# Performance work log

Measured on AMD Instinct MI355X. Metric: run time of the kernel, lower is better.

## Reference

```python
import jax, jax.numpy as jnp
import numpy as np

B, D, H, HD, P, O, K = 256, 1024, 8, 128, 2048, 1024, 4
HID = H * HD
EPS = 1e-5


def setup_inputs() -> dict:
    key = jax.random.key(0)
    ks = jax.random.split(key, 16)

    def w(k, shape, fan_in):
        return jax.random.normal(k, shape, jnp.float32) / np.sqrt(fan_in).astype(np.float32)

    return dict(
        seq=jax.random.normal(ks[0], (B, D), jnp.float32),
        c_tm1=jnp.zeros((B, H, HD, HD), jnp.float32),
        n_tm1=jnp.ones((B, H, HD), jnp.float32),
        m_tm1=jnp.zeros((B, H), jnp.float32),
        ln_g=jnp.ones((D,), jnp.float32), ln_b=jnp.zeros((D,), jnp.float32),
        gn_g=jnp.ones((HID,), jnp.float32), gn_b=jnp.zeros((HID,), jnp.float32),
        W_upl=w(ks[1], (P, D), D), b_upl=jnp.zeros((P,), jnp.float32),
        W_upr=w(ks[2], (HID, D), D), b_upr=jnp.zeros((HID,), jnp.float32),
        W_down=w(ks[3], (D, HID), HID), b_down=jnp.zeros((D,), jnp.float32),
        W_last=w(ks[4], (O, D), D), b_last=jnp.zeros((O,), jnp.float32),
        conv_w=w(ks[5], (K,), K), conv_b=jnp.zeros((), jnp.float32),
        W_skip=w(ks[6], (HID, P), P),
        W_i=w(ks[7], (H, P), P), b_i=jnp.zeros((H,), jnp.float32),
        W_f=w(ks[8], (H, P), P), b_f=jnp.zeros((H,), jnp.float32),
        W_o=w(ks[9], (HID, P), P), b_o=jnp.zeros((HID,), jnp.float32),
        W_q=w(ks[10], (HID, P), P), b_q=jnp.zeros((HID,), jnp.float32),
        W_k=w(ks[11], (HID, P), P), b_k=jnp.zeros((HID,), jnp.float32),
        W_v=w(ks[12], (HID, P), P), b_v=jnp.zeros((HID,), jnp.float32),
    )


def reference(seq, c_tm1, n_tm1, m_tm1, ln_g, ln_b, gn_g, gn_b,
              W_upl, b_upl, W_upr, b_upr, W_down, b_down, W_last, b_last,
              conv_w, conv_b, W_skip, W_i, b_i, W_f, b_f, W_o, b_o,
              W_q, b_q, W_k, b_k, W_v, b_v):
    b = seq.shape[0]
    h, hd = c_tm1.shape[1], c_tm1.shape[2]

    # input LayerNorm
    mu = jnp.mean(seq, -1, keepdims=True)
    var = jnp.var(seq, -1, keepdims=True)
    x_n = (seq - mu) * jax.lax.rsqrt(var + EPS) * ln_g + ln_b

    x_t = x_n @ W_upl.T + b_upl            # [b, P]
    r_t = x_n @ W_upr.T + b_upr            # [b, HID]

    # causal conv over the feature axis (in=out=1 channel), left pad K-1
    k_sz = conv_w.shape[0]
    p = x_t.shape[1]
    xp = jnp.pad(x_t, ((0, 0), (k_sz - 1, 0)))
    x_c = conv_b + sum(conv_w[j] * xp[:, j:j + p] for j in range(k_sz))
    x_c = jax.nn.silu(x_c)                 # [b, P]

    q_t = (x_c @ W_q.T + b_q).reshape(b, h, hd)
    k_t = ((x_c @ W_k.T + b_k) / np.sqrt(hd).astype(np.float32)).reshape(b, h, hd)
    v_t = (x_t @ W_v.T + b_v).reshape(b, h, hd)

    i_t = x_c @ W_i.T + b_i                # [b, h]
    f_t = x_c @ W_f.T + b_f                # [b, h]
    o_t = jax.nn.sigmoid(x_t @ W_o.T + b_o)  # [b, HID]

    # stabilized exponential gating
    m_t = jnp.maximum(f_t + m_tm1, i_t)
    i_g = jnp.exp(i_t - m_t)
    f_g = jnp.exp(f_t - m_t + m_tm1)

    # matrix-memory covariance update
    c_t = f_g[:, :, None, None] * c_tm1 + i_g[:, :, None, None] * jnp.einsum('bhd,bhp->bhdp', v_t, k_t)
    n_t = f_g[:, :, None] * n_tm1 + i_g[:, :, None] * k_t

    num = jnp.einsum('bhdp,bhp->bhd', c_t, q_t)
    den = jnp.maximum(jnp.einsum('bhd,bhd->bh', n_t, q_t), 1.0)
    h_t = o_t * (num / den[:, :, None]).reshape(b, h * hd)

    # GroupNorm(head_num groups) over hidden
    hg = h_t.reshape(b, h, hd)
    gmu = jnp.mean(hg, -1, keepdims=True)
    gvar = jnp.var(hg, -1, keepdims=True)
    hn = ((hg - gmu) * jax.lax.rsqrt(gvar + EPS)).reshape(b, h * hd) * gn_g + gn_b

    out = hn + x_c @ W_skip.T              # 1x1 conv skip == matmul
    out = out * jax.nn.silu(r_t)
    out = out @ W_down.T + b_down
    final = (out + x_n) @ W_last.T + b_last
    return final, c_t, n_t, m_t
```

## Files before the change

### kernel.cpp

```cpp
#include <hip/hip_runtime.h>
#include <cstdint>
#include <cstddef>

#define LN_EPS 1e-5f

typedef float  f32x4  __attribute__((ext_vector_type(4)));
typedef __bf16 bf16x8 __attribute__((ext_vector_type(8)));
typedef unsigned short u16x4 __attribute__((ext_vector_type(4)));

__device__ __forceinline__ float block_sum(float v, volatile float* red) {
#pragma unroll
  for (int o = 32; o > 0; o >>= 1) v += __shfl_down(v, o, 64);
  const int lane = threadIdx.x & 63, w = threadIdx.x >> 6;
  __syncthreads();
  if (lane == 0) red[w] = v;
  __syncthreads();
  return red[0] + red[1] + red[2] + red[3];
}

__global__ __launch_bounds__(256)
void k_ln(const float* __restrict__ seq, const float* __restrict__ g,
          const float* __restrict__ b, float* __restrict__ xn) {
  __shared__ float red[8];
  const int row = blockIdx.x, t = threadIdx.x;
  const f32x4 x = ((const f32x4*)(seq + (size_t)row * 1024))[t];
  float s  = x[0] + x[1] + x[2] + x[3];
  float s2 = x[0]*x[0] + x[1]*x[1] + x[2]*x[2] + x[3]*x[3];
#pragma unroll
  for (int o = 32; o > 0; o >>= 1) { s += __shfl_down(s, o, 64); s2 += __shfl_down(s2, o, 64); }
  const int lane = t & 63, w = t >> 6;
  if (lane == 0) { red[w] = s; red[4 + w] = s2; }
  __syncthreads();
  s  = red[0] + red[1] + red[2] + red[3];
  s2 = red[4] + red[5] + red[6] + red[7];
  const float mu  = s * (1.f / 1024.f);
  const float inv = rsqrtf(s2 * (1.f / 1024.f) - mu * mu + LN_EPS);
  const f32x4 gg = ((const f32x4*)g)[t];
  const f32x4 bb = ((const f32x4*)b)[t];
  f32x4 y;
#pragma unroll
  for (int i = 0; i < 4; ++i) y[i] = (x[i] - mu) * inv * gg[i] + bb[i];
  ((f32x4*)(xn + (size_t)row * 1024))[t] = y;
}

__global__ __launch_bounds__(256)
void k_conv(const float* __restrict__ xt, const float* __restrict__ cw,
            const float* __restrict__ cb, float* __restrict__ xc) {
  __shared__ float s[2048];
  const int row = blockIdx.x, t = threadIdx.x;
  const f32x4* src = (const f32x4*)(xt + (size_t)row * 2048);
  ((f32x4*)s)[t] = src[t];
  ((f32x4*)s)[t + 256] = src[t + 256];
  const float w0 = cw[0], w1 = cw[1], w2 = cw[2], w3 = cw[3], b = cb[0];
  __syncthreads();
  float out[8];
  const int c0 = t * 8;
#pragma unroll
  for (int j = 0; j < 8; ++j) {
    const int c = c0 + j;
    float a = b + w3 * s[c];
    if (c >= 1) a += w2 * s[c - 1];
    if (c >= 2) a += w1 * s[c - 2];
    if (c >= 3) a += w0 * s[c - 3];
    a = a / (1.f + __expf(-a));
    out[j] = a;
  }
  f32x4* dst = (f32x4*)(xc + (size_t)row * 2048 + c0);
  f32x4 v0 = {out[0], out[1], out[2], out[3]};
  f32x4 v1 = {out[4], out[5], out[6], out[7]};
  dst[0] = v0; dst[1] = v1;
}

__global__ __launch_bounds__(256)
void k_if(const float* __restrict__ xc, const float* __restrict__ Wi,
          const float* __restrict__ bi, const float* __restrict__ Wf,
          const float* __restrict__ bfp, const float* __restrict__ m_tm1,
          float* __restrict__ m_out, float* __restrict__ ig, float* __restrict__ fg) {
  __shared__ float sx[2048];
  __shared__ float so[16];
  const int row = blockIdx.x, t = threadIdx.x;
  const f32x4* src = (const f32x4*)(xc + (size_t)row * 2048);
  ((f32x4*)sx)[t] = src[t];
  ((f32x4*)sx)[t + 256] = src[t + 256];
  __syncthreads();
  const int w = t >> 6, lane = t & 63;
  float p[4];
#pragma unroll
  for (int i = 0; i < 4; ++i) {
    const int o = w * 4 + i;
    const float* wr = (o < 8) ? (Wi + (size_t)o * 2048) : (Wf + (size_t)(o - 8) * 2048);
    float acc = 0.f;
#pragma unroll
    for (int j = 0; j < 8; ++j) {
      const f32x4 xv = ((const f32x4*)sx)[j * 64 + lane];
      const f32x4 wv = ((const f32x4*)wr)[j * 64 + lane];
      acc += xv[0]*wv[0] + xv[1]*wv[1] + xv[2]*wv[2] + xv[3]*wv[3];
    }
    p[i] = acc;
  }
#pragma unroll
  for (int i = 0; i < 4; ++i) {
#pragma unroll
    for (int o = 32; o > 0; o >>= 1) p[i] += __shfl_xor(p[i], o, 64);
  }
  if (lane == 0) {
#pragma unroll
    for (int i = 0; i < 4; ++i) so[w * 4 + i] = p[i];
  }
  __syncthreads();
  if (t < 8) {
    const float it = so[t] + bi[t];
    const float ft = so[t + 8] + bfp[t];
    const float mp = m_tm1[row * 8 + t];
    const float m = fmaxf(ft + mp, it);
    m_out[row * 8 + t] = m;
    ig[row * 8 + t] = __expf(it - m);
    fg[row * 8 + t] = __expf(ft - m + mp);
  }
}

__global__ __launch_bounds__(256, 4)
void k_rec(const float* __restrict__ c_tm1, const float* __restrict__ n_tm1,
           const float* __restrict__ qb, const float* __restrict__ kb,
           const float* __restrict__ vb, const float* __restrict__ ot,
           const float* __restrict__ ig, const float* __restrict__ fg,
           const float* __restrict__ gn_g, const float* __restrict__ gn_b,
           const float* __restrict__ skipb, const float* __restrict__ sr,
           float* __restrict__ c_out, float* __restrict__ n_out,
           float* __restrict__ uf) {
  __shared__ float sk[128], sq[128], sv[128], snum[128];
  __shared__ float red[4];
  const int bh = blockIdx.x;
  const int b = bh >> 3, h = bh & 7;
  const int t = threadIdx.x;
  const size_t base = (size_t)b * 1024 + h * 128;
  if (t < 128) { sk[t] = kb[base + t]; sv[t] = vb[base + t]; }
  else         { sq[t - 128] = qb[base + t - 128]; }
  __syncthreads();
  const float fgv = fg[bh], igv = ig[bh];
  const f32x4* C0 = (const f32x4*)(c_tm1 + (size_t)bh * 16384);
  f32x4* Ct = (f32x4*)(c_out + (size_t)bh * 16384);
  const int r0 = t >> 5, c4 = t & 31;
  const f32x4 k4 = ((const f32x4*)sk)[c4];
  const f32x4 q4 = ((const f32x4*)sq)[c4];
  float pd[16];
  f32x4 st[8];
#pragma unroll
  for (int p = 0; p < 8; ++p) st[p] = C0[(p * 8 + r0) * 32 + c4];
#pragma unroll
  for (int g = 0; g < 2; ++g) {
#pragma unroll
    for (int p = 0; p < 8; ++p) {
      const int pass = g * 8 + p;
      const int d = pass * 8 + r0;
      const f32x4 c0v = st[p];
      if (g == 0) st[p] = C0[((8 + p) * 8 + r0) * 32 + c4];
      const float iv = igv * sv[d];
      f32x4 ct = fgv * c0v + iv * k4;
      __builtin_nontemporal_store(ct, Ct + d * 32 + c4);
      pd[pass] = ct[0] * q4[0] + ct[1] * q4[1] + ct[2] * q4[2] + ct[3] * q4[3];
    }
  }
#pragma unroll
  for (int pass = 0; pass < 16; ++pass) {
    float p = pd[pass];
    p += __shfl_xor(p, 1, 64); p += __shfl_xor(p, 2, 64); p += __shfl_xor(p, 4, 64);
    p += __shfl_xor(p, 8, 64); p += __shfl_xor(p, 16, 64);
    pd[pass] = p;
  }
  if (c4 == 0) {
#pragma unroll
    for (int pass = 0; pass < 16; ++pass) snum[pass * 8 + r0] = pd[pass];
  }
  float denp = 0.f, ntd = 0.f;
  if (t < 128) {
    ntd = fgv * n_tm1[(size_t)bh * 128 + t] + igv * sk[t];
    n_out[(size_t)bh * 128 + t] = ntd;
    denp = ntd * sq[t];
  }
  const float den = fmaxf(block_sum(denp, red), 1.f);
  float hv = 0.f;
  if (t < 128) {
    const float o = 1.f / (1.f + __expf(-ot[base + t]));
    hv = o * snum[t] / den;
  }
  const float mu  = block_sum(hv, red) * (1.f / 128.f);
  const float var = block_sum(hv * hv, red) * (1.f / 128.f) - mu * mu;
  if (t < 128) {
    const int hid = h * 128 + t;
    const float hn = (hv - mu) * rsqrtf(var + LN_EPS) * gn_g[hid] + gn_b[hid];
    uf[base + t] = (hn + skipb[base + t]) * sr[base + t];
  }
}

struct GemmSeg {
  const float* A; const float* W; const float* bias; float* out;
  const float* add; int ldOut; int colOfs; int epi; float scale;
};
struct GemmArgs { GemmSeg seg[5]; };

__global__ __launch_bounds__(256)
void k_gemm(int K, GemmArgs ga) {
  __shared__ __align__(16) char lds[2][32768];
  const int tid = threadIdx.x;
  const int lane = tid & 63;
  const int wid = tid >> 6;
  const int wm = wid >> 1;
  const int wn = wid & 1;
  const int segId = blockIdx.x >> 4;
  const int n0 = (blockIdx.x & 15) * 64;
  const int m0 = blockIdx.y * 64;
  const GemmSeg sg = ga.seg[segId];

  const int lrow = tid >> 4;
  const int col4 = tid & 15;

  f32x4 acc[2][2] = {};

  const float* Abase = sg.A + (size_t)m0 * K;
  const float* Wbase = sg.W + (size_t)n0 * K;
  const int NT = K >> 6;

  f32x4 va[4], vw[4], va2[4], vw2[4];
#pragma unroll
  for (int p = 0; p < 4; ++p) {
    const int r = p * 16 + lrow;
    va[p] = *(const f32x4*)(Abase + (size_t)r * K + col4 * 4);
    vw[p] = *(const f32x4*)(Wbase + (size_t)r * K + col4 * 4);
  }

  for (int kt = 0; kt < NT; ++kt) {
    {
      char* lb = lds[kt & 1];
      const int byte = ((((col4 >> 1) ^ (lrow & 7)) << 4) | ((col4 & 1) << 3));
#pragma unroll
      for (int p = 0; p < 4; ++p) {
        const int r = p * 16 + lrow;
        u16x4 ah, al, wh, wl;
#pragma unroll
        for (int i = 0; i < 4; ++i) {
          const unsigned ab = __float_as_uint(va[p][i]);
          const float fh = __uint_as_float(ab & 0xFFFF0000u);
          ah[i] = (unsigned short)(ab >> 16);
          al[i] = (unsigned short)(__float_as_uint(va[p][i] - fh) >> 16);
          const unsigned wb2 = __float_as_uint(vw[p][i]);
          const float wfh = __uint_as_float(wb2 & 0xFFFF0000u);
          wh[i] = (unsigned short)(wb2 >> 16);
          wl[i] = (unsigned short)(__float_as_uint(vw[p][i] - wfh) >> 16);
        }
        *(u16x4*)(lb + r * 128 + byte) = ah;
        *(u16x4*)(lb + 8192 + r * 128 + byte) = al;
        *(u16x4*)(lb + 16384 + r * 128 + byte) = wh;
        *(u16x4*)(lb + 24576 + r * 128 + byte) = wl;
      }
    }
    if (kt + 1 < NT) {
      const int ko = (kt + 1) * 64;
#pragma unroll
      for (int p = 0; p < 4; ++p) {
        const int r = p * 16 + lrow;
        va2[p] = *(const f32x4*)(Abase + (size_t)r * K + ko + col4 * 4);
        vw2[p] = *(const f32x4*)(Wbase + (size_t)r * K + ko + col4 * 4);
      }
    }
    __syncthreads();
    {
      const char* lb = lds[kt & 1];
      const int rA = wm * 32 + (lane & 15);
      const int rB = wn * 32 + (lane & 15);
      const int kg = lane >> 4;
      const int swz = lane & 7;
#pragma unroll
      for (int kk = 0; kk < 2; ++kk) {
        const int so = ((kk * 4 + kg) ^ swz) << 4;
        const char* pa0 = lb + rA * 128 + so;
        const char* pa1 = lb + (rA + 16) * 128 + so;
        const char* pb0 = lb + 16384 + rB * 128 + so;
        const char* pb1 = lb + 16384 + (rB + 16) * 128 + so;
        const bf16x8 ah0 = *(const bf16x8*)(pa0);
        const bf16x8 al0 = *(const bf16x8*)(pa0 + 8192);
        const bf16x8 ah1 = *(const bf16x8*)(pa1);
        const bf16x8 al1 = *(const bf16x8*)(pa1 + 8192);
        const bf16x8 bh0 = *(const bf16x8*)(pb0);
        const bf16x8 bl0 = *(const bf16x8*)(pb0 + 8192);
        const bf16x8 bh1 = *(const bf16x8*)(pb1);
        const bf16x8 bl1 = *(const bf16x8*)(pb1 + 8192);
        acc[0][0] = __builtin_amdgcn_mfma_f32_16x16x32_bf16(ah0, bh0, acc[0][0], 0, 0, 0);
        acc[0][1] = __builtin_amdgcn_mfma_f32_16x16x32_bf16(ah0, bh1, acc[0][1], 0, 0, 0);
        acc[1][0] = __builtin_amdgcn_mfma_f32_16x16x32_bf16(ah1, bh0, acc[1][0], 0, 0, 0);
        acc[1][1] = __builtin_amdgcn_mfma_f32_16x16x32_bf16(ah1, bh1, acc[1][1], 0, 0, 0);
        acc[0][0] = __builtin_amdgcn_mfma_f32_16x16x32_bf16(ah0, bl0, acc[0][0], 0, 0, 0);
        acc[0][1] = __builtin_amdgcn_mfma_f32_16x16x32_bf16(ah0, bl1, acc[0][1], 0, 0, 0);
        acc[1][0] = __builtin_amdgcn_mfma_f32_16x16x32_bf16(ah1, bl0, acc[1][0], 0, 0, 0);
        acc[1][1] = __builtin_amdgcn_mfma_f32_16x16x32_bf16(ah1, bl1, acc[1][1], 0, 0, 0);
        acc[0][0] = __builtin_amdgcn_mfma_f32_16x16x32_bf16(al0, bh0, acc[0][0], 0, 0, 0);
        acc[0][1] = __builtin_amdgcn_mfma_f32_16x16x32_bf16(al0, bh1, acc[0][1], 0, 0, 0);
        acc[1][0] = __builtin_amdgcn_mfma_f32_16x16x32_bf16(al1, bh0, acc[1][0], 0, 0, 0);
        acc[1][1] = __builtin_amdgcn_mfma_f32_16x16x32_bf16(al1, bh1, acc[1][1], 0, 0, 0);
      }
    }
#pragma unroll
    for (int p = 0; p < 4; ++p) { va[p] = va2[p]; vw[p] = vw2[p]; }
    __syncthreads();
  }

  const int rowb = m0 + wm * 32 + (lane >> 4) * 4;
  const int colb = n0 + wn * 32 + (lane & 15);
#pragma unroll
  for (int mf = 0; mf < 2; ++mf) {
#pragma unroll
    for (int nf = 0; nf < 2; ++nf) {
      const int col = colb + nf * 16;
      const float bv = sg.bias ? sg.bias[col] : 0.f;
#pragma unroll
      for (int i = 0; i < 4; ++i) {
        const int row = rowb + mf * 16 + i;
        float v = acc[mf][nf][i] + bv;
        if (sg.epi == 1)      v = v / (1.f + __expf(-v));
        else if (sg.epi == 3) v *= sg.scale;
        else if (sg.epi == 4) v += sg.add[(size_t)row * 1024 + col];
        sg.out[(size_t)row * sg.ldOut + sg.colOfs + col] = v;
      }
    }
  }
}

extern "C" void kernel_launch(void* const* d_in, const int* in_sizes, int n_in,
                              void* d_out, int out_size, void* d_ws, size_t ws_size,
                              hipStream_t stream) {
  (void)in_sizes; (void)n_in; (void)out_size; (void)ws_size;
  const float* seq    = (const float*)d_in[0];
  const float* c_tm1  = (const float*)d_in[1];
  const float* n_tm1  = (const float*)d_in[2];
  const float* m_tm1  = (const float*)d_in[3];
  const float* ln_g   = (const float*)d_in[4];
  const float* ln_b   = (const float*)d_in[5];
  const float* gn_g   = (const float*)d_in[6];
  const float* gn_b   = (const float*)d_in[7];
  const float* W_upl  = (const float*)d_in[8];
  const float* b_upl  = (const float*)d_in[9];
  const float* W_upr  = (const float*)d_in[10];
  const float* b_upr  = (const float*)d_in[11];
  const float* W_down = (const float*)d_in[12];
  const float* b_down = (const float*)d_in[13];
  const float* W_last = (const float*)d_in[14];
  const float* b_last = (const float*)d_in[15];
  const float* conv_w = (const float*)d_in[16];
  const float* conv_b = (const float*)d_in[17];
  const float* W_skip = (const float*)d_in[18];
  const float* W_i    = (const float*)d_in[19];
  const float* b_i    = (const float*)d_in[20];
  const float* W_f    = (const float*)d_in[21];
  const float* b_f    = (const float*)d_in[22];
  const float* W_o    = (const float*)d_in[23];
  const float* b_o    = (const float*)d_in[24];
  const float* W_q    = (const float*)d_in[25];
  const float* b_q    = (const float*)d_in[26];
  const float* W_k    = (const float*)d_in[27];
  const float* b_k    = (const float*)d_in[28];
  const float* W_v    = (const float*)d_in[29];
  const float* b_v    = (const float*)d_in[30];

  float* out_final = (float*)d_out;
  float* out_c = out_final + (size_t)256 * 1024;
  float* out_n = out_c + (size_t)256 * 8 * 128 * 128;
  float* out_m = out_n + (size_t)256 * 8 * 128;

  char* ws = (char*)d_ws;
  size_t off = 0;
  auto alloc = [&](size_t bytes) -> void* {
    void* p = ws + off; off += (bytes + 255) & ~(size_t)255; return p;
  };
  float* x_n   = (float*)alloc((size_t)256 * 1024 * 4);
  float* x_t   = (float*)alloc((size_t)256 * 2048 * 4);
  float* sr    = (float*)alloc((size_t)256 * 1024 * 4);
  float* x_c   = (float*)alloc((size_t)256 * 2048 * 4);
  float* qb    = (float*)alloc((size_t)256 * 1024 * 4);
  float* kb    = (float*)alloc((size_t)256 * 1024 * 4);
  float* vb    = (float*)alloc((size_t)256 * 1024 * 4);
  float* otb   = (float*)alloc((size_t)256 * 1024 * 4);
  float* skipb = (float*)alloc((size_t)256 * 1024 * 4);
  float* igb   = (float*)alloc((size_t)2048 * 4);
  float* fgb   = (float*)alloc((size_t)2048 * 4);
  float* u_f   = (float*)alloc((size_t)256 * 1024 * 4);
  float* t_f   = (float*)alloc((size_t)256 * 1024 * 4);

  k_ln<<<256, 256, 0, stream>>>(seq, ln_g, ln_b, x_n);

  GemmArgs gA = {};
  gA.seg[0] = {x_n, W_upl, b_upl, x_t, nullptr, 2048, 0, 0, 0.f};
  gA.seg[1] = {x_n, W_upl + (size_t)1024 * 1024, b_upl + 1024, x_t, nullptr, 2048, 1024, 0, 0.f};
  gA.seg[2] = {x_n, W_upr, b_upr, sr, nullptr, 1024, 0, 1, 0.f};
  k_gemm<<<dim3(48, 4), 256, 0, stream>>>(1024, gA);

  k_conv<<<256, 256, 0, stream>>>(x_t, conv_w, conv_b, x_c);

  k_if<<<256, 256, 0, stream>>>(x_c, W_i, b_i, W_f, b_f, m_tm1, out_m, igb, fgb);

  GemmArgs gBC = {};
  gBC.seg[0] = {x_c, W_q, b_q, qb, nullptr, 1024, 0, 0, 0.f};
  gBC.seg[1] = {x_c, W_k, b_k, kb, nullptr, 1024, 0, 3, 0.08838834764831845f};
  gBC.seg[2] = {x_c, W_skip, nullptr, skipb, nullptr, 1024, 0, 0, 0.f};
  gBC.seg[3] = {x_t, W_v, b_v, vb, nullptr, 1024, 0, 0, 0.f};
  gBC.seg[4] = {x_t, W_o, b_o, otb, nullptr, 1024, 0, 0, 0.f};
  k_gemm<<<dim3(80, 4), 256, 0, stream>>>(2048, gBC);

  k_rec<<<2048, 256, 0, stream>>>(c_tm1, n_tm1, qb, kb, vb, otb, igb, fgb,
                                  gn_g, gn_b, skipb, sr, out_c, out_n, u_f);

  GemmArgs gD = {};
  gD.seg[0] = {u_f, W_down, b_down, t_f, x_n, 1024, 0, 4, 0.f};
  k_gemm<<<dim3(16, 4), 256, 0, stream>>>(1024, gD);

  GemmArgs gE = {};
  gE.seg[0] = {t_f, W_last, b_last, out_final, nullptr, 1024, 0, 0, 0.f};
  k_gemm<<<dim3(16, 4), 256, 0, stream>>>(1024, gE);
}
```

Before: 162.0 us.

## Add split-K to GEMMs, fuse conv with gate kernel, restructure recurrence loads

All GEMM launches now split the K dimension across blockIdx.z (2 or 4 ways). Partial tiles go to a workspace buffer, and the last-arriving block, found through an atomic counter, reduces them and runs the epilogue. The goal is more parallelism for the small-grid GEMMs, especially the 64-block down and last projections. The conv and i/f gate kernels are merged so x_c stays in LDS instead of being re-read, and the recurrence kernel now loads all C rows up front with nontemporal loads and reads v/k/q directly from global memory. The costs are extra workspace traffic, atomics, a memset launch, and higher register pressure in the recurrence kernel.

```diff
diff --git a/kernel.cpp b/kernel.cpp
--- a/kernel.cpp
+++ b/kernel.cpp
@@ -44,9 +44,15 @@
 }
 
 __global__ __launch_bounds__(256)
-void k_conv(const float* __restrict__ xt, const float* __restrict__ cw,
-            const float* __restrict__ cb, float* __restrict__ xc) {
+void k_conv_if(const float* __restrict__ xt, const float* __restrict__ cw,
+               const float* __restrict__ cb, float* __restrict__ xc,
+               const float* __restrict__ Wi, const float* __restrict__ bi,
+               const float* __restrict__ Wf, const float* __restrict__ bfp,
+               const float* __restrict__ m_tm1, float* __restrict__ m_out,
+               float* __restrict__ ig, float* __restrict__ fg) {
   __shared__ float s[2048];
+  __shared__ float sx[2048];
+  __shared__ float so[16];
   const int row = blockIdx.x, t = threadIdx.x;
   const f32x4* src = (const f32x4*)(xt + (size_t)row * 2048);
   ((f32x4*)s)[t] = src[t];
@@ -65,23 +71,12 @@
     a = a / (1.f + __expf(-a));
     out[j] = a;
   }
-  f32x4* dst = (f32x4*)(xc + (size_t)row * 2048 + c0);
   f32x4 v0 = {out[0], out[1], out[2], out[3]};
   f32x4 v1 = {out[4], out[5], out[6], out[7]};
+  f32x4* dst = (f32x4*)(xc + (size_t)row * 2048 + c0);
   dst[0] = v0; dst[1] = v1;
-}
-
-__global__ __launch_bounds__(256)
-void k_if(const float* __restrict__ xc, const float* __restrict__ Wi,
-          const float* __restrict__ bi, const float* __restrict__ Wf,
-          const float* __restrict__ bfp, const float* __restrict__ m_tm1,
-          float* __restrict__ m_out, float* __restrict__ ig, float* __restrict__ fg) {
-  __shared__ float sx[2048];
-  __shared__ float so[16];
-  const int row = blockIdx.x, t = threadIdx.x;
-  const f32x4* src = (const f32x4*)(xc + (size_t)row * 2048);
-  ((f32x4*)sx)[t] = src[t];
-  ((f32x4*)sx)[t + 256] = src[t + 256];
+  ((f32x4*)sx)[t * 2] = v0;
+  ((f32x4*)sx)[t * 2 + 1] = v1;
   __syncthreads();
   const int w = t >> 6, lane = t & 63;
   float p[4];
@@ -119,64 +114,87 @@
   }
 }
 
-__global__ __launch_bounds__(256, 4)
-void k_rec(const float* __restrict__ c_tm1, const float* __restrict__ n_tm1,
-           const float* __restrict__ qb, const float* __restrict__ kb,
-           const float* __restrict__ vb, const float* __restrict__ ot,
-           const float* __restrict__ ig, const float* __restrict__ fg,
-           const float* __restrict__ gn_g, const float* __restrict__ gn_b,
-           const float* __restrict__ skipb, const float* __restrict__ sr,
-           float* __restrict__ c_out, float* __restrict__ n_out,
-           float* __restrict__ uf) {
-  __shared__ float sk[128], sq[128], sv[128], snum[128];
+__global__ __launch_bounds__(256)
+void k_rec_all(const float* __restrict__ c_tm1, const float* __restrict__ n_tm1,
+               const float* __restrict__ qb, const float* __restrict__ kb,
+               const float* __restrict__ vb, const float* __restrict__ ot,
+               const float* __restrict__ ig, const float* __restrict__ fg,
+               const float* __restrict__ gn_g, const float* __restrict__ gn_b,
+               const float* __restrict__ skipb, const float* __restrict__ sr,
+               float* __restrict__ c_out, float* __restrict__ n_out,
+               float* __restrict__ uf) {
+  __shared__ float snum[128];
   __shared__ float red[4];
   const int bh = blockIdx.x;
   const int b = bh >> 3, h = bh & 7;
   const int t = threadIdx.x;
+  const int w = t >> 6, lane = t & 63;
+  const int c4 = lane & 31;
+  const int half = lane >> 5;
   const size_t base = (size_t)b * 1024 + h * 128;
-  if (t < 128) { sk[t] = kb[base + t]; sv[t] = vb[base + t]; }
-  else         { sq[t - 128] = qb[base + t - 128]; }
-  __syncthreads();
   const float fgv = fg[bh], igv = ig[bh];
+  const f32x4 k4 = ((const f32x4*)(kb + base))[c4];
+  const f32x4 q4 = ((const f32x4*)(qb + base))[c4];
   const f32x4* C0 = (const f32x4*)(c_tm1 + (size_t)bh * 16384);
   f32x4* Ct = (f32x4*)(c_out + (size_t)bh * 16384);
-  const int r0 = t >> 5, c4 = t & 31;
-  const f32x4 k4 = ((const f32x4*)sk)[c4];
-  const f32x4 q4 = ((const f32x4*)sq)[c4];
+  const int row0 = w * 32;
+  f32x4 st0[8], st1[8]; float vr0[8], vr1[8];
+#pragma unroll
+  for (int p = 0; p < 8; ++p) {
+    const int r = row0 + 2 * p + half;
+    st0[p] = __builtin_nontemporal_load(C0 + r * 32 + c4);
+    vr0[p] = vb[base + r];
+  }
+#pragma unroll
+  for (int p = 0; p < 8; ++p) {
+    const int r = row0 + 16 + 2 * p + half;
+    st1[p] = __builtin_nontemporal_load(C0 + r * 32 + c4);
+    vr1[p] = vb[base + r];
+  }
+#pragma unroll
+  for (int p = 0; p < 8; ++p)
+    asm volatile("" : "+v"(st0[p][0]), "+v"(st0[p][1]), "+v"(st0[p][2]), "+v"(st0[p][3]));
   float pd[16];
-  f32x4 st[8];
-#pragma unroll
-  for (int p = 0; p < 8; ++p) st[p] = C0[(p * 8 + r0) * 32 + c4];
-#pragma unroll
-  for (int g = 0; g < 2; ++g) {
-#pragma unroll
-    for (int p = 0; p < 8; ++p) {
-      const int pass = g * 8 + p;
-      const int d = pass * 8 + r0;
-      const f32x4 c0v = st[p];
-      if (g == 0) st[p] = C0[((8 + p) * 8 + r0) * 32 + c4];
-      const float iv = igv * sv[d];
-      f32x4 ct = fgv * c0v + iv * k4;
-      __builtin_nontemporal_store(ct, Ct + d * 32 + c4);
-      pd[pass] = ct[0] * q4[0] + ct[1] * q4[1] + ct[2] * q4[2] + ct[3] * q4[3];
-    }
-  }
-#pragma unroll
-  for (int pass = 0; pass < 16; ++pass) {
-    float p = pd[pass];
+#pragma unroll
+  for (int p = 0; p < 8; ++p) {
+    const int r = row0 + 2 * p + half;
+    const float iv = igv * vr0[p];
+    f32x4 ct = fgv * st0[p] + iv * k4;
+    Ct[r * 32 + c4] = ct;
+    pd[p] = ct[0] * q4[0] + ct[1] * q4[1] + ct[2] * q4[2] + ct[3] * q4[3];
+  }
+#pragma unroll
+  for (int p = 0; p < 8; ++p)
+    asm volatile("" : "+v"(st1[p][0]), "+v"(st1[p][1]), "+v"(st1[p][2]), "+v"(st1[p][3]));
+#pragma unroll
+  for (int p = 0; p < 8; ++p) {
+    const int r = row0 + 16 + 2 * p + half;
+    const float iv = igv * vr1[p];
+    f32x4 ct = fgv * st1[p] + iv * k4;
+    Ct[r * 32 + c4] = ct;
+    pd[8 + p] = ct[0] * q4[0] + ct[1] * q4[1] + ct[2] * q4[2] + ct[3] * q4[3];
+  }
+#pragma unroll
+  for (int j = 0; j < 16; ++j) {
+    float p = pd[j];
     p += __shfl_xor(p, 1, 64); p += __shfl_xor(p, 2, 64); p += __shfl_xor(p, 4, 64);
     p += __shfl_xor(p, 8, 64); p += __shfl_xor(p, 16, 64);
-    pd[pass] = p;
+    pd[j] = p;
   }
   if (c4 == 0) {
 #pragma unroll
-    for (int pass = 0; pass < 16; ++pass) snum[pass * 8 + r0] = pd[pass];
-  }
+    for (int j = 0; j < 16; ++j) {
+      const int r = row0 + ((j < 8) ? (2 * j) : (2 * j)) + half;
+      snum[(j < 8) ? (row0 + 2 * j + half) : (row0 + 16 + 2 * (j - 8) + half)] = pd[j];
+      (void)r;
+    }
+  }
+  __syncthreads();
   float denp = 0.f, ntd = 0.f;
   if (t < 128) {
-    ntd = fgv * n_tm1[(size_t)bh * 128 + t] + igv * sk[t];
+    ntd = fgv * n_tm1[(size_t)bh * 128 + t] + igv * kb[base + t];
     n_out[(size_t)bh * 128 + t] = ntd;
-    denp = ntd * sq[t];
+    denp = ntd * qb[base + t];
   }
   const float den = fmaxf(block_sum(denp, red), 1.f);
   float hv = 0.f;
@@ -197,11 +215,12 @@
   const float* A; const float* W; const float* bias; float* out;
   const float* add; int ldOut; int colOfs; int epi; float scale;
 };
-struct GemmArgs { GemmSeg seg[5]; };
+struct GemmArgs { GemmSeg seg[5]; int splitk; float* pbuf; int* ctr; };
 
 __global__ __launch_bounds__(256)
 void k_gemm(int K, GemmArgs ga) {
   __shared__ __align__(16) char lds[2][32768];
+  __shared__ int sOld;
   const int tid = threadIdx.x;
   const int lane = tid & 63;
   const int wid = tid >> 6;
@@ -210,16 +229,20 @@
   const int segId = blockIdx.x >> 4;
   const int n0 = (blockIdx.x & 15) * 64;
   const int m0 = blockIdx.y * 64;
+  const int kc = blockIdx.z;
   const GemmSeg sg = ga.seg[segId];
+
+  const int chunk = K / ga.splitk;
+  const int Kbase = kc * chunk;
+  const int NT = chunk >> 6;
 
   const int lrow = tid >> 4;
   const int col4 = tid & 15;
 
   f32x4 acc[2][2] = {};
 
-  const float* Abase = sg.A + (size_t)m0 * K;
-  const float* Wbase = sg.W + (size_t)n0 * K;
-  const int NT = K >> 6;
+  const float* Abase = sg.A + (size_t)m0 * K + Kbase;
+  const float* Wbase = sg.W + (size_t)n0 * K + Kbase;
 
   f32x4 va[4], vw[4], va2[4], vw2[4];
 #pragma unroll
@@ -304,6 +327,49 @@
     __syncthreads();
   }
 
+  const int rowT = wm * 32 + (lane >> 4) * 4;
+  const int colT = wn * 32 + (lane & 15);
+  f32x4 accF[2][2];
+
+  if (ga.splitk > 1) {
+    const int tile = blockIdx.x * 4 + blockIdx.y;
+    float* pb = ga.pbuf + ((size_t)tile * ga.splitk + kc) * 4096;
+#pragma unroll
+    for (int mf = 0; mf < 2; ++mf)
+#pragma unroll
+      for (int nf = 0; nf < 2; ++nf)
+#pragma unroll
+        for (int i = 0; i < 4; ++i)
+          __hip_atomic_store(&pb[(rowT + mf * 16 + i) * 64 + colT + nf * 16],
+                             acc[mf][nf][i], __ATOMIC_RELAXED, __HIP_MEMORY_SCOPE_AGENT);
+    __threadfence();
+    __syncthreads();
+    if (tid == 0)
+      sOld = __hip_atomic_fetch_add(&ga.ctr[tile], 1, __ATOMIC_ACQ_REL, __HIP_MEMORY_SCOPE_AGENT);
+    __syncthreads();
+    if (sOld != ga.splitk - 1) return;
+    __threadfence();
+    const float* pb0 = ga.pbuf + (size_t)tile * ga.splitk * 4096;
+#pragma unroll
+    for (int mf = 0; mf < 2; ++mf)
+#pragma unroll
+      for (int nf = 0; nf < 2; ++nf)
+#pragma unroll
+        for (int i = 0; i < 4; ++i) {
+          float sum = 0.f;
+          const int pos = (rowT + mf * 16 + i) * 64 + colT + nf * 16;
+          for (int sK = 0; sK < ga.splitk; ++sK)
+            sum += __hip_atomic_load(&pb0[sK * 4096 + pos], __ATOMIC_RELAXED, __HIP_MEMORY_SCOPE_AGENT);
+          accF[mf][nf][i] = sum;
+        }
+  } else {
+#pragma unroll
+    for (int mf = 0; mf < 2; ++mf)
+#pragma unroll
+      for (int nf = 0; nf < 2; ++nf)
+        accF[mf][nf] = acc[mf][nf];
+  }
+
   const int rowb = m0 + wm * 32 + (lane >> 4) * 4;
   const int colb = n0 + wn * 32 + (lane & 15);
 #pragma unroll
@@ -315,7 +381,7 @@
 #pragma unroll
       for (int i = 0; i < 4; ++i) {
         const int row = rowb + mf * 16 + i;
-        float v = acc[mf][nf][i] + bv;
+        float v = accF[mf][nf][i] + bv;
         if (sg.epi == 1)      v = v / (1.f + __expf(-v));
         else if (sg.epi == 3) v *= sg.scale;
         else if (sg.epi == 4) v += sg.add[(size_t)row * 1024 + col];
@@ -384,6 +450,13 @@
   float* fgb   = (float*)alloc((size_t)2048 * 4);
   float* u_f   = (float*)alloc((size_t)256 * 1024 * 4);
   float* t_f   = (float*)alloc((size_t)256 * 1024 * 4);
+  int*   ctrs  = (int*)alloc((size_t)704 * 4);
+  float* pbufA = (float*)alloc((size_t)192 * 2 * 4096 * 4);
+  float* pbufBC= (float*)alloc((size_t)320 * 2 * 4096 * 4);
+  float* pbufD = (float*)alloc((size_t)64 * 4 * 4096 * 4);
+  float* pbufE = (float*)alloc((size_t)64 * 4 * 4096 * 4);
+
+  hipMemsetAsync(ctrs, 0, 704 * 4, stream);
 
   k_ln<<<256, 256, 0, stream>>>(seq, ln_g, ln_b, x_n);
 
@@ -391,11 +464,11 @@
   gA.seg[0] = {x_n, W_upl, b_upl, x_t, nullptr, 2048, 0, 0, 0.f};
   gA.seg[1] = {x_n, W_upl + (size_t)1024 * 1024, b_upl + 1024, x_t, nullptr, 2048, 1024, 0, 0.f};
   gA.seg[2] = {x_n, W_upr, b_upr, sr, nullptr, 1024, 0, 1, 0.f};
-  k_gemm<<<dim3(48, 4), 256, 0, stream>>>(1024, gA);
-
-  k_conv<<<256, 256, 0, stream>>>(x_t, conv_w, conv_b, x_c);
-
-  k_if<<<256, 256, 0, stream>>>(x_c, W_i, b_i, W_f, b_f, m_tm1, out_m, igb, fgb);
+  gA.splitk = 2; gA.pbuf = pbufA; gA.ctr = ctrs;
+  k_gemm<<<dim3(48, 4, 2), 256, 0, stream>>>(1024, gA);
+
+  k_conv_if<<<256, 256, 0, stream>>>(x_t, conv_w, conv_b, x_c,
+                                     W_i, b_i, W_f, b_f, m_tm1, out_m, igb, fgb);
 
   GemmArgs gBC = {};
   gBC.seg[0] = {x_c, W_q, b_q, qb, nullptr, 1024, 0, 0, 0.f};
@@ -403,16 +476,19 @@
   gBC.seg[2] = {x_c, W_skip, nullptr, skipb, nullptr, 1024, 0, 0, 0.f};
   gBC.seg[3] = {x_t, W_v, b_v, vb, nullptr, 1024, 0, 0, 0.f};
   gBC.seg[4] = {x_t, W_o, b_o, otb, nullptr, 1024, 0, 0, 0.f};
-  k_gemm<<<dim3(80, 4), 256, 0, stream>>>(2048, gBC);
-
-  k_rec<<<2048, 256, 0, stream>>>(c_tm1, n_tm1, qb, kb, vb, otb, igb, fgb,
-                                  gn_g, gn_b, skipb, sr, out_c, out_n, u_f);
+  gBC.splitk = 2; gBC.pbuf = pbufBC; gBC.ctr = ctrs + 192;
+  k_gemm<<<dim3(80, 4, 2), 256, 0, stream>>>(2048, gBC);
+
+  k_rec_all<<<2048, 256, 0, stream>>>(c_tm1, n_tm1, qb, kb, vb, otb, igb, fgb,
+                                      gn_g, gn_b, skipb, sr, out_c, out_n, u_f);
 
   GemmArgs gD = {};
   gD.seg[0] = {u_f, W_down, b_down, t_f, x_n, 1024, 0, 4, 0.f};
-  k_gemm<<<dim3(16, 4), 256, 0, stream>>>(1024, gD);
+  gD.splitk = 4; gD.pbuf = pbufD; gD.ctr = ctrs + 512;
+  k_gemm<<<dim3(16, 4, 4), 256, 0, stream>>>(1024, gD);
 
   GemmArgs gE = {};
   gE.seg[0] = {t_f, W_last, b_last, out_final, nullptr, 1024, 0, 0, 0.f};
-  k_gemm<<<dim3(16, 4), 256, 0, stream>>>(1024, gE);
-}
+  gE.splitk = 4; gE.pbuf = pbufE; gE.ctr = ctrs + 576;
+  k_gemm<<<dim3(16, 4, 4), 256, 0, stream>>>(1024, gE);
+}
```

New measurement: 347.5 us. 2.15x slower.
